# Kernel optimization log

Hardware: AMD Instinct MI355X
Metric: run time of the kernel (lower is better)

The kernel has to match this reference:

```python
import jax, jax.numpy as jnp
import numpy as np

N_NODES = 50000
NEG_SLOPE = 0.2


def _gat_conv(x, edge_index, W, att_src, att_dst, bias, heads, out_ch, concat):
    """PyG-style GATConv (add_self_loops=True, negative_slope=0.2).
    x: [N, F_in], edge_index: [2, E] (row=src, row=dst), W: [F_in, heads*out_ch],
    att_src/att_dst: [heads, out_ch], bias: [heads*out_ch] or [out_ch]."""
    N = x.shape[0]
    # add self-loops
    loops = jnp.arange(N, dtype=edge_index.dtype)
    src = jnp.concatenate([edge_index[0], loops])
    dst = jnp.concatenate([edge_index[1], loops])

    h = (x @ W).reshape(N, heads, out_ch)                 # [N, H, C]
    a_src = jnp.einsum('nhc,hc->nh', h, att_src)          # [N, H]
    a_dst = jnp.einsum('nhc,hc->nh', h, att_dst)          # [N, H]

    e = a_src[src] + a_dst[dst]                           # [E', H]
    e = jnp.where(e >= 0, e, NEG_SLOPE * e)               # leaky_relu

    # segment softmax over incoming edges of each dst node
    e_max = jax.ops.segment_max(e, dst, num_segments=N)   # [N, H]
    e_max = jnp.where(jnp.isfinite(e_max), e_max, 0.0)
    ex = jnp.exp(e - e_max[dst])                          # [E', H]
    denom = jax.ops.segment_sum(ex, dst, num_segments=N)  # [N, H]
    alpha = ex / (denom[dst] + 1e-16)                     # [E', H]

    msg = alpha[:, :, None] * h[src]                      # [E', H, C]
    out = jax.ops.segment_sum(msg, dst, num_segments=N)   # [N, H, C]

    if concat:
        out = out.reshape(N, heads * out_ch)
    else:
        out = out.mean(axis=1)
    return out + bias


def setup_inputs() -> dict:
    key = jax.random.key(0)
    ks = jax.random.split(key, 12)
    F_in, hid, H1, C, H2 = 512, 8, 8, 40, 1
    x = jax.random.normal(ks[0], (N_NODES, F_in), dtype=jnp.float32)
    edge_index = jax.random.randint(ks[1], (2, 1600000), 0, N_NODES, dtype=jnp.int64)
    s1 = 1.0 / np.sqrt(F_in)
    s2 = 1.0 / np.sqrt(hid * H1)
    return {
        'x': x,
        'edge_index': edge_index,
        'W1': jax.random.normal(ks[2], (F_in, H1 * hid), dtype=jnp.float32) * s1,
        'att_src1': jax.random.normal(ks[3], (H1, hid), dtype=jnp.float32) * s2,
        'att_dst1': jax.random.normal(ks[4], (H1, hid), dtype=jnp.float32) * s2,
        'b1': jnp.zeros((H1 * hid,), dtype=jnp.float32),
        'W2': jax.random.normal(ks[5], (H1 * hid, H2 * C), dtype=jnp.float32) * s2,
        'att_src2': jax.random.normal(ks[6], (H2, C), dtype=jnp.float32) * 0.15,
        'att_dst2': jax.random.normal(ks[7], (H2, C), dtype=jnp.float32) * 0.15,
        'b2': jnp.zeros((C,), dtype=jnp.float32),
    }


def reference(x, edge_index, W1, att_src1, att_dst1, b1, W2, att_src2, att_dst2, b2):
    # eval mode: dropout is identity
    h = _gat_conv(x, edge_index, W1, att_src1, att_dst1, b1, heads=8, out_ch=8, concat=True)
    h = jax.nn.relu(h)
    h = _gat_conv(h, edge_index, W2, att_src2, att_dst2, b2, heads=1, out_ch=40, concat=False)
    return jax.nn.log_softmax(h, axis=1)
```

## Files before the change

kernel.cpp:

```cpp
#include <hip/hip_runtime.h>
#include <math.h>

#define NNODES 50000
#define NEG_SLOPE 0.2f
#define NB 391
#define BW 128
#define CHUNK 4096
#define CAP 8128

typedef __bf16 bf16x8 __attribute__((ext_vector_type(8)));
typedef float f32x4 __attribute__((ext_vector_type(4)));

__global__ void prep(const float* __restrict__ W1, __bf16* __restrict__ W1b,
                     int* __restrict__ bcur) {
    int i = blockIdx.x * 256 + threadIdx.x;
    if (i < NB) bcur[i] = i * CAP;
    else if (i == NB) bcur[NB] = 0;
    if (i >= 512 * 64) return;
    int k = i >> 6, n = i & 63;
    W1b[((size_t)(k >> 3) * 64 + n) * 8 + (k & 7)] = (__bf16)W1[i];
}

__global__ __launch_bounds__(256) void bin_scatter(const int* __restrict__ ei,
                                                   int E, int N, int* bcur,
                                                   int* __restrict__ tmp) {
    __shared__ int lcnt[NB];
    __shared__ int lbase[NB];
    int tid = threadIdx.x;
    int base0 = blockIdx.x * CHUNK;
    int lim = min(base0 + CHUNK, E + N);
    for (int i = tid; i < NB; i += 256) lcnt[i] = 0;
    __syncthreads();
    for (int e = base0 + tid; e < lim; e += 256) {
        int d = (e < E) ? ei[E + e] : e - E;
        atomicAdd(&lcnt[d >> 7], 1);
    }
    __syncthreads();
    for (int b = tid; b < NB; b += 256) {
        int c = lcnt[b];
        lbase[b] = c ? atomicAdd(&bcur[b], c) : 0;
    }
    __syncthreads();
    for (int i = tid; i < NB; i += 256) lcnt[i] = 0;
    __syncthreads();
    for (int e = base0 + tid; e < lim; e += 256) {
        int s, d;
        if (e < E) { s = ei[e]; d = ei[E + e]; }
        else       { s = d = e - E; }
        int b = d >> 7;
        int p = atomicAdd(&lcnt[b], 1);
        tmp[lbase[b] + p] = ((d & 127) << 16) | s;
    }
}

__global__ __launch_bounds__(256) void csr_finalize(int* __restrict__ bcur,
                                                    const int* __restrict__ tmp,
                                                    int N, int* __restrict__ off,
                                                    int* __restrict__ off_end,
                                                    int* __restrict__ slot) {
    __shared__ int cnt[BW];
    __shared__ int cur[BW];
    __shared__ int cbase_s;
    int b = blockIdx.x, tid = threadIdx.x;
    int base = b * CAP;
    int m = bcur[b] - base;
    if (tid < BW) cnt[tid] = 0;
    __syncthreads();
    for (int i = tid; i < m; i += 256)
        atomicAdd(&cnt[(tmp[base + i] >> 16) & 127], 1);
    __syncthreads();
    if (tid == 0) cbase_s = atomicAdd(&bcur[NB], m);
    int myv = (tid < BW) ? cnt[tid] : 0;
    for (int o = 1; o < BW; o <<= 1) {
        int u = 0;
        if (tid >= o && tid < BW) u = cnt[tid - o];
        __syncthreads();
        if (tid < BW) cnt[tid] += u;
        __syncthreads();
    }
    if (tid < BW) {
        int ex = cbase_s + cnt[tid] - myv;
        cur[tid] = ex;
        int g = b * BW + tid;
        if (g < N) { off[g] = ex; off_end[g] = ex + myv; }
    }
    __syncthreads();
    for (int i = tid; i < m; i += 256) {
        int v = tmp[base + i];
        int k = (v >> 16) & 127;
        int p = atomicAdd(&cur[k], 1);
        slot[p] = v & 0xFFFF;
    }
}

__global__ __launch_bounds__(256) void gemm1_mfma(const float* __restrict__ X,
                                                  const __bf16* __restrict__ W1b,
                                                  const float* __restrict__ att_s1,
                                                  const float* __restrict__ att_d1,
                                                  __bf16* __restrict__ H1b,
                                                  float* __restrict__ a_s1,
                                                  float* __restrict__ a_d1,
                                                  int M) {
    __shared__ __bf16 As[2048];
    __shared__ __bf16 Bs[2048];
    int tid = threadIdx.x, wid = tid >> 6, lane = tid & 63;
    int quad = lane >> 4, l15 = lane & 15;
    int m0 = blockIdx.x * 64;
    f32x4 acc[4] = {{0.f, 0.f, 0.f, 0.f}, {0.f, 0.f, 0.f, 0.f},
                    {0.f, 0.f, 0.f, 0.f}, {0.f, 0.f, 0.f, 0.f}};
    int mrow = tid >> 2;
    int kq_w = tid & 3;
    int xrow = min(m0 + mrow, M - 1);
    const float* xp = X + (size_t)xrow * 512 + kq_w * 8;
    for (int kb = 0; kb < 16; ++kb) {
        float4 xa = *(const float4*)(xp + kb * 32);
        float4 xb = *(const float4*)(xp + kb * 32 + 4);
        bf16x8 av;
        av[0] = (__bf16)xa.x; av[1] = (__bf16)xa.y;
        av[2] = (__bf16)xa.z; av[3] = (__bf16)xa.w;
        av[4] = (__bf16)xb.x; av[5] = (__bf16)xb.y;
        av[6] = (__bf16)xb.z; av[7] = (__bf16)xb.w;
        *(bf16x8*)(As + ((size_t)kq_w * 64 + mrow) * 8) = av;
        *(bf16x8*)(Bs + ((size_t)wid * 64 + lane) * 8) =
            *(const bf16x8*)(W1b + ((size_t)(kb * 4 + wid) * 64 + lane) * 8);
        __syncthreads();
        bf16x8 af = *(const bf16x8*)(As + ((size_t)quad * 64 + 16 * wid + l15) * 8);
#pragma unroll
        for (int t = 0; t < 4; ++t) {
            bf16x8 bf = *(const bf16x8*)(Bs + ((size_t)quad * 64 + 16 * t + l15) * 8);
            acc[t] = __builtin_amdgcn_mfma_f32_16x16x32_bf16(af, bf, acc[t], 0, 0, 0);
        }
        __syncthreads();
    }
    float asv[4], adv[4];
#pragma unroll
    for (int t = 0; t < 4; ++t) {
        asv[t] = att_s1[16 * t + l15];
        adv[t] = att_d1[16 * t + l15];
    }
#pragma unroll
    for (int t = 0; t < 4; ++t) {
#pragma unroll
        for (int r = 0; r < 4; ++r) {
            int gm = m0 + 16 * wid + quad * 4 + r;
            if (gm < M) H1b[(size_t)gm * 64 + 16 * t + l15] = (__bf16)acc[t][r];
            float ps = acc[t][r] * asv[t];
            float pd = acc[t][r] * adv[t];
            ps += __shfl_xor(ps, 1); ps += __shfl_xor(ps, 2); ps += __shfl_xor(ps, 4);
            pd += __shfl_xor(pd, 1); pd += __shfl_xor(pd, 2); pd += __shfl_xor(pd, 4);
            if (gm < M && (l15 & 7) == 0) {
                int hh = 2 * t + (l15 >> 3);
                a_s1[(size_t)gm * 8 + hh] = ps;
                a_d1[(size_t)gm * 8 + hh] = pd;
            }
        }
    }
}

__global__ __launch_bounds__(256) void agg1_fused(const int* __restrict__ off,
                                                  const int* __restrict__ off_end,
                                                  const int* __restrict__ slot,
                                                  const __bf16* __restrict__ H1b,
                                                  const float* __restrict__ a_src,
                                                  const float* __restrict__ a_dst,
                                                  const float* __restrict__ b1,
                                                  const float* __restrict__ W2,
                                                  const float* __restrict__ att_src2,
                                                  const float* __restrict__ att_dst2,
                                                  __bf16* __restrict__ H2b,
                                                  float* __restrict__ a_s2,
                                                  float* __restrict__ a_d2) {
    __shared__ float W2s[64 * 40];
    __shared__ float rows[4][64];
    int tid = threadIdx.x;
    int wid = tid >> 6, lane = tid & 63;
    for (int i = tid; i < 64 * 40; i += 256) W2s[i] = W2[i];
    __syncthreads();
    int d = blockIdx.x * 4 + wid;
    int beg = off[d], end = off_end[d];
    int h = lane >> 3;
    int eh = lane & 7;
    int es = lane >> 3;
    float adst_c = a_dst[(size_t)d * 8 + eh];
    float acc = 0.f, den_l = 0.f;
    for (int i = beg; i < end; i += 8) {
        int j = i + es;
        int jj = (j < end) ? j : (end - 1);
        int s = slot[jj];
        float e = a_src[(size_t)s * 8 + eh] + adst_c;
        e = (e >= 0.f) ? e : NEG_SLOPE * e;
        float w = (j < end) ? __expf(e) : 0.f;
        den_l += w;
#pragma unroll
        for (int q = 0; q < 8; ++q) {
            int sq = __builtin_amdgcn_readlane(s, q << 3);
            float wq = __shfl(w, (q << 3) | h);
            acc += wq * (float)H1b[(size_t)sq * 64 + lane];
        }
    }
    den_l += __shfl_xor(den_l, 8);
    den_l += __shfl_xor(den_l, 16);
    den_l += __shfl_xor(den_l, 32);
    float den = __shfl(den_l, h);
    float v = acc / (den + 1e-16f) + b1[lane];
    v = (v > 0.f) ? v : 0.f;
    rows[wid][lane] = v;
    int c = lane, cc = (c < 40) ? c : 0;
    float acc2 = 0.f;
    const float* rp = rows[wid];
#pragma unroll 8
    for (int k = 0; k < 64; ++k) acc2 += rp[k] * W2s[k * 40 + cc];
    if (c < 40) H2b[(size_t)d * 40 + c] = (__bf16)acc2;
    float ps = (c < 40) ? acc2 * att_src2[cc] : 0.f;
    float pd = (c < 40) ? acc2 * att_dst2[cc] : 0.f;
#pragma unroll
    for (int mm = 32; mm >= 1; mm >>= 1) {
        ps += __shfl_xor(ps, mm);
        pd += __shfl_xor(pd, mm);
    }
    if (lane == 0) { a_s2[d] = ps; a_d2[d] = pd; }
}

__global__ __launch_bounds__(256) void agg2(const int* __restrict__ off,
                                            const int* __restrict__ off_end,
                                            const int* __restrict__ slot,
                                            const __bf16* __restrict__ H2b,
                                            const float* __restrict__ a_src2,
                                            const float* __restrict__ a_d2,
                                            const float* __restrict__ b2,
                                            float* __restrict__ out) {
    int wid = threadIdx.x >> 6, lane = threadIdx.x & 63;
    int d = blockIdx.x * 4 + wid;
    int beg = off[d], end = off_end[d];
    float adst = a_d2[d];
    int c = lane;
    int cc = (c < 40) ? c : 0;
    float acc = 0.f, den = 0.f;
    for (int i = beg; i < end; i += 64) {
        int j = i + lane;
        int jj = (j < end) ? j : (end - 1);
        int s = slot[jj];
        float e = a_src2[s] + adst;
        e = (e >= 0.f) ? e : NEG_SLOPE * e;
        float w = (j < end) ? __expf(e) : 0.f;
        den += w;
#pragma unroll
        for (int qb = 0; qb < 8; ++qb) {
            if (i + (qb << 3) >= end) break;
#pragma unroll
            for (int qq = 0; qq < 8; ++qq) {
                int q = (qb << 3) + qq;
                int sq = __builtin_amdgcn_readlane(s, q);
                float wq = __uint_as_float(
                    __builtin_amdgcn_readlane((int)__float_as_uint(w), q));
                acc += wq * (float)H2b[(size_t)sq * 40 + cc];
            }
        }
    }
#pragma unroll
    for (int m = 32; m >= 1; m >>= 1) den += __shfl_xor(den, m);
    float v = acc / (den + 1e-16f) + b2[cc];
    float vm = (c < 40) ? v : -3.0e38f;
#pragma unroll
    for (int m = 32; m >= 1; m >>= 1) vm = fmaxf(vm, __shfl_xor(vm, m));
    float se = (c < 40) ? __expf(v - vm) : 0.f;
#pragma unroll
    for (int m = 32; m >= 1; m >>= 1) se += __shfl_xor(se, m);
    float res = v - vm - __logf(se);
    if (c < 40) out[(size_t)d * 40 + c] = res;
}

extern "C" void kernel_launch(void* const* d_in, const int* in_sizes, int n_in,
                              void* d_out, int out_size, void* d_ws, size_t ws_size,
                              hipStream_t stream) {
    const float* x   = (const float*)d_in[0];
    const int*   ei  = (const int*)d_in[1];
    const float* W1  = (const float*)d_in[2];
    const float* as1 = (const float*)d_in[3];
    const float* ad1 = (const float*)d_in[4];
    const float* b1  = (const float*)d_in[5];
    const float* W2  = (const float*)d_in[6];
    const float* as2 = (const float*)d_in[7];
    const float* ad2 = (const float*)d_in[8];
    const float* b2  = (const float*)d_in[9];
    float* out = (float*)d_out;

    const int N = NNODES;
    const int E = in_sizes[1] / 2;
    const int total = E + N;

    char* ws = (char*)d_ws;
    size_t o = 0;
    auto alloc = [&](size_t bytes) -> void* {
        void* p = ws + o;
        o = (o + bytes + 255) & ~(size_t)255;
        return p;
    };
    int* bcur    = (int*)alloc((size_t)(NB + 1) * 4);
    int* off     = (int*)alloc((size_t)N * 4);
    int* off_end = (int*)alloc((size_t)N * 4);
    int* slot    = (int*)alloc((size_t)total * 4);
    int* tmp     = (int*)alloc((size_t)NB * CAP * 4);
    __bf16* W1b = (__bf16*)alloc((size_t)512 * 64 * 2);
    __bf16* H1b = (__bf16*)alloc((size_t)N * 64 * 2);
    float* a_s1 = (float*)alloc((size_t)N * 8 * 4);
    float* a_d1 = (float*)alloc((size_t)N * 8 * 4);
    __bf16* H2b = (__bf16*)alloc((size_t)N * 40 * 2);
    float* a_s2 = (float*)alloc((size_t)N * 4);
    float* a_d2 = (float*)alloc((size_t)N * 4);
    (void)ws_size; (void)n_in; (void)out_size;

    prep<<<(512 * 64 + 255) / 256, 256, 0, stream>>>(W1, W1b, bcur);
    bin_scatter<<<(total + CHUNK - 1) / CHUNK, 256, 0, stream>>>(ei, E, N, bcur, tmp);
    csr_finalize<<<NB, 256, 0, stream>>>(bcur, tmp, N, off, off_end, slot);

    gemm1_mfma<<<(N + 63) / 64, 256, 0, stream>>>(x, W1b, as1, ad1, H1b, a_s1, a_d1, N);

    agg1_fused<<<N / 4, 256, 0, stream>>>(off, off_end, slot, H1b, a_s1, a_d1, b1,
                                          W2, as2, ad2, H2b, a_s2, a_d2);

    agg2<<<N / 4, 256, 0, stream>>>(off, off_end, slot, H2b, a_s2, a_d2, b2, out);
}
```

Measured before the change: 352.8 us.

## Restructure GAT aggregations so each lane gathers a 16-byte vector per edge

Both aggregation kernels now give each group of 8 lanes one edge and each lane an 8-element bf16 vector load of the source row, accumulating 8 values per lane and reducing across edge groups with xor shuffles at the end. Previously lanes did scalar bf16 gathers with per-edge readlane and shuffle broadcasts. The layer-2 feature matrix is padded to 64 columns so rows are aligned for vector loads. The layer-2 projection reads activations through readlane instead of shared memory, and log-softmax uses an 8-lane reduction with vectorized stores. The padding adds extra bytes per row to the layer-2 gathers and more registers per thread.

```diff
diff --git a/kernel.cpp b/kernel.cpp
--- a/kernel.cpp
+++ b/kernel.cpp
@@ -10,6 +10,10 @@
 
 typedef __bf16 bf16x8 __attribute__((ext_vector_type(8)));
 typedef float f32x4 __attribute__((ext_vector_type(4)));
+
+__device__ inline float rlane(float v, int l) {
+    return __uint_as_float(__builtin_amdgcn_readlane((int)__float_as_uint(v), l));
+}
 
 __global__ void prep(const float* __restrict__ W1, __bf16* __restrict__ W1b,
                      int* __restrict__ bcur) {
@@ -171,18 +175,19 @@
                                                   float* __restrict__ a_s2,
                                                   float* __restrict__ a_d2) {
     __shared__ float W2s[64 * 40];
-    __shared__ float rows[4][64];
     int tid = threadIdx.x;
     int wid = tid >> 6, lane = tid & 63;
     for (int i = tid; i < 64 * 40; i += 256) W2s[i] = W2[i];
     __syncthreads();
     int d = blockIdx.x * 4 + wid;
     int beg = off[d], end = off_end[d];
-    int h = lane >> 3;
+    int es = lane >> 3;
     int eh = lane & 7;
-    int es = lane >> 3;
     float adst_c = a_dst[(size_t)d * 8 + eh];
-    float acc = 0.f, den_l = 0.f;
+    const __bf16* hbase = H1b + eh * 8;
+    float acc[8] = {0.f, 0.f, 0.f, 0.f, 0.f, 0.f, 0.f, 0.f};
+    float den_l = 0.f;
+#pragma unroll 2
     for (int i = beg; i < end; i += 8) {
         int j = i + es;
         int jj = (j < end) ? j : (end - 1);
@@ -191,26 +196,34 @@
         e = (e >= 0.f) ? e : NEG_SLOPE * e;
         float w = (j < end) ? __expf(e) : 0.f;
         den_l += w;
-#pragma unroll
-        for (int q = 0; q < 8; ++q) {
-            int sq = __builtin_amdgcn_readlane(s, q << 3);
-            float wq = __shfl(w, (q << 3) | h);
-            acc += wq * (float)H1b[(size_t)sq * 64 + lane];
-        }
-    }
-    den_l += __shfl_xor(den_l, 8);
-    den_l += __shfl_xor(den_l, 16);
-    den_l += __shfl_xor(den_l, 32);
-    float den = __shfl(den_l, h);
-    float v = acc / (den + 1e-16f) + b1[lane];
-    v = (v > 0.f) ? v : 0.f;
-    rows[wid][lane] = v;
+        bf16x8 hv = *(const bf16x8*)(hbase + (size_t)s * 64);
+#pragma unroll
+        for (int q = 0; q < 8; ++q) acc[q] += w * (float)hv[q];
+    }
+#pragma unroll
+    for (int m = 8; m <= 32; m <<= 1) {
+        den_l += __shfl_xor(den_l, m);
+#pragma unroll
+        for (int q = 0; q < 8; ++q) acc[q] += __shfl_xor(acc[q], m);
+    }
+    float rden = 1.f / (den_l + 1e-16f);
+    float vr[8];
+#pragma unroll
+    for (int q = 0; q < 8; ++q) {
+        float t = acc[q] * rden + b1[eh * 8 + q];
+        vr[q] = (t > 0.f) ? t : 0.f;
+    }
     int c = lane, cc = (c < 40) ? c : 0;
-    float acc2 = 0.f;
-    const float* rp = rows[wid];
-#pragma unroll 8
-    for (int k = 0; k < 64; ++k) acc2 += rp[k] * W2s[k * 40 + cc];
-    if (c < 40) H2b[(size_t)d * 40 + c] = (__bf16)acc2;
+    float acc2a = 0.f, acc2b = 0.f;
+#pragma unroll
+    for (int k = 0; k < 64; k += 2) {
+        float r0 = rlane(vr[k & 7], k >> 3);
+        float r1 = rlane(vr[(k + 1) & 7], (k + 1) >> 3);
+        acc2a += r0 * W2s[k * 40 + cc];
+        acc2b += r1 * W2s[(k + 1) * 40 + cc];
+    }
+    float acc2 = acc2a + acc2b;
+    H2b[(size_t)d * 64 + c] = (__bf16)((c < 40) ? acc2 : 0.f);
     float ps = (c < 40) ? acc2 * att_src2[cc] : 0.f;
     float pd = (c < 40) ? acc2 * att_dst2[cc] : 0.f;
 #pragma unroll
@@ -229,45 +242,60 @@
                                             const float* __restrict__ a_d2,
                                             const float* __restrict__ b2,
                                             float* __restrict__ out) {
-    int wid = threadIdx.x >> 6, lane = threadIdx.x & 63;
+    int tid = threadIdx.x;
+    int wid = tid >> 6, lane = tid & 63;
     int d = blockIdx.x * 4 + wid;
     int beg = off[d], end = off_end[d];
+    int es = lane >> 3;
+    int sl = lane & 7;
     float adst = a_d2[d];
-    int c = lane;
-    int cc = (c < 40) ? c : 0;
-    float acc = 0.f, den = 0.f;
-    for (int i = beg; i < end; i += 64) {
-        int j = i + lane;
+    const __bf16* hbase = H2b + sl * 8;
+    bool valid = (sl < 5);
+    float acc[8] = {0.f, 0.f, 0.f, 0.f, 0.f, 0.f, 0.f, 0.f};
+    float den_l = 0.f;
+#pragma unroll 2
+    for (int i = beg; i < end; i += 8) {
+        int j = i + es;
         int jj = (j < end) ? j : (end - 1);
         int s = slot[jj];
         float e = a_src2[s] + adst;
         e = (e >= 0.f) ? e : NEG_SLOPE * e;
         float w = (j < end) ? __expf(e) : 0.f;
-        den += w;
-#pragma unroll
-        for (int qb = 0; qb < 8; ++qb) {
-            if (i + (qb << 3) >= end) break;
-#pragma unroll
-            for (int qq = 0; qq < 8; ++qq) {
-                int q = (qb << 3) + qq;
-                int sq = __builtin_amdgcn_readlane(s, q);
-                float wq = __uint_as_float(
-                    __builtin_amdgcn_readlane((int)__float_as_uint(w), q));
-                acc += wq * (float)H2b[(size_t)sq * 40 + cc];
-            }
-        }
-    }
-#pragma unroll
-    for (int m = 32; m >= 1; m >>= 1) den += __shfl_xor(den, m);
-    float v = acc / (den + 1e-16f) + b2[cc];
-    float vm = (c < 40) ? v : -3.0e38f;
-#pragma unroll
-    for (int m = 32; m >= 1; m >>= 1) vm = fmaxf(vm, __shfl_xor(vm, m));
-    float se = (c < 40) ? __expf(v - vm) : 0.f;
-#pragma unroll
-    for (int m = 32; m >= 1; m >>= 1) se += __shfl_xor(se, m);
-    float res = v - vm - __logf(se);
-    if (c < 40) out[(size_t)d * 40 + c] = res;
+        den_l += w;
+        bf16x8 hv = *(const bf16x8*)(hbase + (size_t)s * 64);
+#pragma unroll
+        for (int q = 0; q < 8; ++q) acc[q] += w * (float)hv[q];
+    }
+#pragma unroll
+    for (int m = 8; m <= 32; m <<= 1) {
+        den_l += __shfl_xor(den_l, m);
+#pragma unroll
+        for (int q = 0; q < 8; ++q) acc[q] += __shfl_xor(acc[q], m);
+    }
+    float rden = 1.f / (den_l + 1e-16f);
+    float v[8];
+    float vm = -3.0e38f;
+#pragma unroll
+    for (int q = 0; q < 8; ++q) {
+        v[q] = acc[q] * rden + b2[valid ? sl * 8 + q : 0];
+        vm = fmaxf(vm, v[q]);
+    }
+    if (!valid) vm = -3.0e38f;
+#pragma unroll
+    for (int m = 1; m <= 4; m <<= 1) vm = fmaxf(vm, __shfl_xor(vm, m));
+    float se = 0.f;
+#pragma unroll
+    for (int q = 0; q < 8; ++q) se += __expf(v[q] - vm);
+    if (!valid) se = 0.f;
+#pragma unroll
+    for (int m = 1; m <= 4; m <<= 1) se += __shfl_xor(se, m);
+    float lse = vm + __logf(se);
+    if (es == 0 && valid) {
+        f32x4 o0 = {v[0] - lse, v[1] - lse, v[2] - lse, v[3] - lse};
+        f32x4 o1 = {v[4] - lse, v[5] - lse, v[6] - lse, v[7] - lse};
+        *(f32x4*)(out + (size_t)d * 40 + sl * 8) = o0;
+        *(f32x4*)(out + (size_t)d * 40 + sl * 8 + 4) = o1;
+    }
 }
 
 extern "C" void kernel_launch(void* const* d_in, const int* in_sizes, int n_in,
@@ -305,7 +333,7 @@
     __bf16* H1b = (__bf16*)alloc((size_t)N * 64 * 2);
     float* a_s1 = (float*)alloc((size_t)N * 8 * 4);
     float* a_d1 = (float*)alloc((size_t)N * 8 * 4);
-    __bf16* H2b = (__bf16*)alloc((size_t)N * 40 * 2);
+    __bf16* H2b = (__bf16*)alloc((size_t)N * 64 * 2);
     float* a_s2 = (float*)alloc((size_t)N * 4);
     float* a_d2 = (float*)alloc((size_t)N * 4);
     (void)ws_size; (void)n_in; (void)out_size;
```

Result: no change. 352.2 us (-0.2%).
